# Optimization experiments

Hardware: AMD Instinct MI355X
Metric: run time of the kernel (lower is better)

Reference implementation:

```python
import jax, jax.numpy as jnp
import numpy as np

HIDDEN = 512
LATENT = 256
NUM_NODE_TYPES = 16


def setup_inputs() -> dict:
    key = jax.random.key(0)
    ks = jax.random.split(key, 9)
    s = lambda fan_in: 1.0 / np.sqrt(fan_in)
    return {
        "z": jax.random.normal(ks[0], (1024, LATENT), dtype=jnp.float32),
        "num_nodes": 128,
        "W_z": jax.random.uniform(ks[1], (LATENT, HIDDEN), jnp.float32, -s(LATENT), s(LATENT)),
        "b_z": jax.random.uniform(ks[2], (HIDDEN,), jnp.float32, -s(LATENT), s(LATENT)),
        "W_node": jax.random.uniform(ks[3], (HIDDEN, NUM_NODE_TYPES), jnp.float32, -s(HIDDEN), s(HIDDEN)),
        "b_node": jax.random.uniform(ks[4], (NUM_NODE_TYPES,), jnp.float32, -s(HIDDEN), s(HIDDEN)),
        "W_e1": jax.random.uniform(ks[5], (2 * HIDDEN, HIDDEN), jnp.float32, -s(2 * HIDDEN), s(2 * HIDDEN)),
        "b_e1": jax.random.uniform(ks[6], (HIDDEN,), jnp.float32, -s(2 * HIDDEN), s(2 * HIDDEN)),
        "W_e2": jax.random.uniform(ks[7], (HIDDEN, 1), jnp.float32, -s(HIDDEN), s(HIDDEN)),
        "b_e2": jax.random.uniform(ks[8], (1,), jnp.float32, -s(HIDDEN), s(HIDDEN)),
    }


def reference(z, num_nodes, W_z, b_z, W_node, b_node, W_e1, b_e1, W_e2, b_e2):
    # h: [B, H]
    h = jax.nn.relu(z @ W_z + b_z)
    B = z.shape[0]
    # h_expanded: [B, N, H] (same h replicated per node, as in the original)
    h_expanded = jnp.broadcast_to(h[:, None, :], (B, num_nodes, h.shape[-1]))
    node_logits = h_expanded @ W_node + b_node  # [B, N, T]
    # Every (i, j) pair in the original loop uses cat(h, h) -> identical scalar per batch.
    h_pair = jnp.concatenate([h, h], axis=-1)  # [B, 2H]
    p = jax.nn.sigmoid(jax.nn.relu(h_pair @ W_e1 + b_e1) @ W_e2 + b_e2)  # [B, 1]
    # Scatter onto strict lower triangle (j < i), zeros elsewhere.
    tril = jnp.tril(jnp.ones((num_nodes, num_nodes), dtype=z.dtype), k=-1)  # [N, N]
    edge_probs = p[:, :, None] * tril[None, :, :]  # [B, N, N]
    return node_logits, edge_probs
```

## Files before the change

kernel.cpp:

```cpp
#include <hip/hip_runtime.h>
#include <hip/hip_bf16.h>
#include <math.h>

#define BB 1024
#define LL 256
#define HH 512
#define TT 16
#define NN 128

#define NODE_F4 (BB * NN * TT / 4)
#define EDGE_F4 (BB * NN * NN / 4)

typedef short bf16x8 __attribute__((ext_vector_type(8)));
typedef short s16x4  __attribute__((ext_vector_type(4)));
typedef float f32x4  __attribute__((ext_vector_type(4)));

static __device__ __forceinline__ short bfbits(float f) {
    __hip_bfloat16 h = __float2bfloat16(f);
    return *reinterpret_cast<short*>(&h);
}

__device__ __forceinline__ void transpose_tile(const float* __restrict__ in,
                                               __hip_bfloat16* __restrict__ out,
                                               int k0, int n0, int Kdim, bool fold,
                                               __hip_bfloat16 (*tile)[34]) {
    const int tx = threadIdx.x & 31;
    const int ty = threadIdx.x >> 5;
    #pragma unroll
    for (int r = ty; r < 32; r += 8) {
        float v = in[(k0 + r) * HH + n0 + tx];
        if (fold) v += in[(k0 + r + HH) * HH + n0 + tx];
        tile[r][tx] = __float2bfloat16(v);
    }
    __syncthreads();
    #pragma unroll
    for (int r = ty; r < 32; r += 8) {
        out[(n0 + r) * Kdim + k0 + tx] = tile[tx][r];
    }
}

__global__ __launch_bounds__(256) void k_prep(const float* __restrict__ z,
                                              const float* __restrict__ Wz,
                                              const float* __restrict__ We1,
                                              const float* __restrict__ Wn,
                                              __hip_bfloat16* __restrict__ z_bf,
                                              __hip_bfloat16* __restrict__ WzT,
                                              __hip_bfloat16* __restrict__ WsumT,
                                              __hip_bfloat16* __restrict__ WnT,
                                              float* __restrict__ p_acc) {
    __shared__ __hip_bfloat16 tile[32][34];
    const int bid = blockIdx.x;
    const int tid = threadIdx.x;
    if (bid < 256) {
        const int q = bid * 256 + tid;
        float4 v = ((const float4*)z)[q];
        s16x4 o; o.x = bfbits(v.x); o.y = bfbits(v.y); o.z = bfbits(v.z); o.w = bfbits(v.w);
        ((s16x4*)z_bf)[q] = o;
    } else if (bid < 384) {
        const int t = bid - 256;
        transpose_tile(Wz, WzT, (t >> 4) * 32, (t & 15) * 32, LL, false, tile);
    } else if (bid < 640) {
        const int t = bid - 384;
        transpose_tile(We1, WsumT, (t >> 4) * 32, (t & 15) * 32, HH, true, tile);
    } else if (bid < 672) {
        const int u = (bid - 640) * 256 + tid;
        const int tt = u >> 9, k = u & 511;
        WnT[u] = __float2bfloat16(Wn[k * TT + tt]);
    } else {
        ((float4*)p_acc)[tid] = make_float4(0.f, 0.f, 0.f, 0.f);
    }
}

__global__ __launch_bounds__(256) void k_gemm1(const __hip_bfloat16* __restrict__ A,
                                               const __hip_bfloat16* __restrict__ Bt,
                                               const float* __restrict__ bias,
                                               __hip_bfloat16* __restrict__ out) {
    const int wid  = (blockIdx.x << 2) + (threadIdx.x >> 6);
    const int lane = threadIdx.x & 63;
    const int mt = wid >> 5, nt = wid & 31;
    const int l16 = lane & 15, quad = lane >> 4;

    const short* Ap = (const short*)A  + (mt * 16 + l16) * LL + quad * 8;
    const short* Bp = (const short*)Bt + (nt * 16 + l16) * LL + quad * 8;

    f32x4 acc = {0.f, 0.f, 0.f, 0.f};
    #pragma unroll
    for (int kt = 0; kt < LL / 32; ++kt) {
        bf16x8 a = *(const bf16x8*)(Ap + kt * 32);
        bf16x8 b = *(const bf16x8*)(Bp + kt * 32);
        acc = __builtin_amdgcn_mfma_f32_16x16x32_bf16(a, b, acc, 0, 0, 0);
    }
    const int col = nt * 16 + l16;
    const float bb = bias[col];
    #pragma unroll
    for (int r = 0; r < 4; ++r) {
        out[(mt * 16 + quad * 4 + r) * HH + col] = __float2bfloat16(fmaxf(acc[r] + bb, 0.f));
    }
}

__global__ __launch_bounds__(256) void k_gemm2_phead(const __hip_bfloat16* __restrict__ A,
                                                     const __hip_bfloat16* __restrict__ Bt,
                                                     const float* __restrict__ be1,
                                                     const float* __restrict__ We2,
                                                     float* __restrict__ p_acc) {
    const int wid  = (blockIdx.x << 2) + (threadIdx.x >> 6);
    const int lane = threadIdx.x & 63;
    const int mt = wid >> 5, nt = wid & 31;
    const int l16 = lane & 15, quad = lane >> 4;

    const short* Ap = (const short*)A  + (mt * 16 + l16) * HH + quad * 8;
    const short* Bp = (const short*)Bt + (nt * 16 + l16) * HH + quad * 8;

    f32x4 acc = {0.f, 0.f, 0.f, 0.f};
    #pragma unroll
    for (int kt = 0; kt < HH / 32; ++kt) {
        bf16x8 a = *(const bf16x8*)(Ap + kt * 32);
        bf16x8 b = *(const bf16x8*)(Bp + kt * 32);
        acc = __builtin_amdgcn_mfma_f32_16x16x32_bf16(a, b, acc, 0, 0, 0);
    }
    const int col = nt * 16 + l16;
    const float bb = be1[col];
    const float w2 = We2[col];
    float sr[4];
    #pragma unroll
    for (int r = 0; r < 4; ++r) sr[r] = fmaxf(acc[r] + bb, 0.f) * w2;
    #pragma unroll
    for (int off = 1; off < 16; off <<= 1) {
        #pragma unroll
        for (int r = 0; r < 4; ++r) sr[r] += __shfl_xor(sr[r], off);
    }
    if (l16 == 0) {
        #pragma unroll
        for (int r = 0; r < 4; ++r)
            atomicAdd(p_acc + mt * 16 + quad * 4 + r, sr[r]);
    }
}

__global__ __launch_bounds__(256) void k_small(const __hip_bfloat16* __restrict__ h,
                                               const __hip_bfloat16* __restrict__ WnT,
                                               const float* __restrict__ bn,
                                               const float* __restrict__ p_acc,
                                               const float* __restrict__ be2,
                                               float* __restrict__ node16,
                                               float* __restrict__ p) {
    const int wid  = (blockIdx.x << 2) + (threadIdx.x >> 6);
    const int lane = threadIdx.x & 63;
    const int l16 = lane & 15, quad = lane >> 4;

    const short* Ap = (const short*)h   + (wid * 16 + l16) * HH + quad * 8;
    const short* Bp = (const short*)WnT + l16 * HH + quad * 8;

    f32x4 acc = {0.f, 0.f, 0.f, 0.f};
    #pragma unroll
    for (int kt = 0; kt < HH / 32; ++kt) {
        bf16x8 a = *(const bf16x8*)(Ap + kt * 32);
        bf16x8 b = *(const bf16x8*)(Bp + kt * 32);
        acc = __builtin_amdgcn_mfma_f32_16x16x32_bf16(a, b, acc, 0, 0, 0);
    }
    const float bb = bn[l16];
    #pragma unroll
    for (int r = 0; r < 4; ++r)
        node16[(wid * 16 + quad * 4 + r) * TT + l16] = acc[r] + bb;

    const int idx = blockIdx.x * 256 + threadIdx.x;
    if (idx < BB) {
        float t = p_acc[idx] + be2[0];
        p[idx] = 1.f / (1.f + expf(-t));
    }
}

__global__ __launch_bounds__(256) void k_write(const float* __restrict__ node16,
                                               const float* __restrict__ p,
                                               float4* __restrict__ out) {
    const int q = blockIdx.x * 256 + threadIdx.x;
    if (q < NODE_F4) {
        const int b  = q >> 9;
        const int t4 = q & 3;
        out[q] = ((const float4*)(node16 + b * TT))[t4];
    } else {
        const int e  = q - NODE_F4;
        const int b  = e >> 12;
        const int i  = (e >> 5) & 127;
        const int j0 = (e & 31) * 4;
        const float pv = p[b];
        float4 v;
        v.x = (j0 + 0 < i) ? pv : 0.f;
        v.y = (j0 + 1 < i) ? pv : 0.f;
        v.z = (j0 + 2 < i) ? pv : 0.f;
        v.w = (j0 + 3 < i) ? pv : 0.f;
        out[q] = v;
    }
}

extern "C" void kernel_launch(void* const* d_in, const int* in_sizes, int n_in,
                              void* d_out, int out_size, void* d_ws, size_t ws_size,
                              hipStream_t stream) {
    const float* z    = (const float*)d_in[0];
    const float* Wz   = (const float*)d_in[2];
    const float* bz   = (const float*)d_in[3];
    const float* Wn   = (const float*)d_in[4];
    const float* bn   = (const float*)d_in[5];
    const float* We1  = (const float*)d_in[6];
    const float* be1  = (const float*)d_in[7];
    const float* We2  = (const float*)d_in[8];
    const float* be2  = (const float*)d_in[9];
    float* out = (float*)d_out;

    char* base = (char*)d_ws;
    __hip_bfloat16* z_bf   = (__hip_bfloat16*)(base);
    __hip_bfloat16* WzT    = (__hip_bfloat16*)(base +  512 * 1024);
    __hip_bfloat16* WsumT  = (__hip_bfloat16*)(base +  768 * 1024);
    __hip_bfloat16* WnT    = (__hip_bfloat16*)(base + 1280 * 1024);
    __hip_bfloat16* h_bf   = (__hip_bfloat16*)(base + 1296 * 1024);
    float*          node16 = (float*)(base + 2320 * 1024);
    float*          p_acc  = (float*)(base + 2384 * 1024);
    float*          p      = (float*)(base + 2388 * 1024);

    k_prep<<<673, 256, 0, stream>>>(z, Wz, We1, Wn, z_bf, WzT, WsumT, WnT, p_acc);

    k_gemm1<<<512, 256, 0, stream>>>(z_bf, WzT, bz, h_bf);

    k_gemm2_phead<<<512, 256, 0, stream>>>(h_bf, WsumT, be1, We2, p_acc);

    k_small<<<16, 256, 0, stream>>>(h_bf, WnT, bn, p_acc, be2, node16, p);

    k_write<<<(NODE_F4 + EDGE_F4) / 256, 256, 0, stream>>>(node16, p, (float4*)out);

    (void)in_sizes; (void)n_in; (void)out_size; (void)ws_size;
}
```

Baseline: 128.6 us.

## Fuse both GEMMs, node head and edge head into one per-row-tile kernel

Replaces the separate z-to-bf16 conversion, GEMM1, GEMM2+p-head and small node-head kernels with one kernel. Each 512-thread block owns 16 batch rows, converts z to bf16 in registers, computes h into a swizzled LDS buffer, then runs the node-logit and edge-MLP GEMMs from LDS and reduces partial sums in shared memory instead of with global atomics. This removes three launches, the global round trip for h and z_bf, and the p_acc zeroing and atomics. In exchange only 64 blocks run, so far fewer waves occupy the GPU, and every block re-reads the full weight matrices.

```diff
diff --git a/kernel.cpp b/kernel.cpp
--- a/kernel.cpp
+++ b/kernel.cpp
@@ -12,12 +12,15 @@
 #define EDGE_F4 (BB * NN * NN / 4)
 
 typedef short bf16x8 __attribute__((ext_vector_type(8)));
-typedef short s16x4  __attribute__((ext_vector_type(4)));
 typedef float f32x4  __attribute__((ext_vector_type(4)));
 
 static __device__ __forceinline__ short bfbits(float f) {
     __hip_bfloat16 h = __float2bfloat16(f);
     return *reinterpret_cast<short*>(&h);
+}
+
+static __device__ __forceinline__ int h_addr(int row, int col) {
+    return (row << 10) + ((((col >> 3) ^ (row & 7)) << 4)) + ((col & 7) << 1);
 }
 
 __device__ __forceinline__ void transpose_tile(const float* __restrict__ in,
@@ -39,133 +42,148 @@
     }
 }
 
-__global__ __launch_bounds__(256) void k_prep(const float* __restrict__ z,
-                                              const float* __restrict__ Wz,
+__global__ __launch_bounds__(256) void k_prep(const float* __restrict__ Wz,
                                               const float* __restrict__ We1,
                                               const float* __restrict__ Wn,
-                                              __hip_bfloat16* __restrict__ z_bf,
                                               __hip_bfloat16* __restrict__ WzT,
                                               __hip_bfloat16* __restrict__ WsumT,
-                                              __hip_bfloat16* __restrict__ WnT,
-                                              float* __restrict__ p_acc) {
+                                              __hip_bfloat16* __restrict__ WnT) {
     __shared__ __hip_bfloat16 tile[32][34];
     const int bid = blockIdx.x;
     const int tid = threadIdx.x;
-    if (bid < 256) {
-        const int q = bid * 256 + tid;
-        float4 v = ((const float4*)z)[q];
-        s16x4 o; o.x = bfbits(v.x); o.y = bfbits(v.y); o.z = bfbits(v.z); o.w = bfbits(v.w);
-        ((s16x4*)z_bf)[q] = o;
+    if (bid < 128) {
+        transpose_tile(Wz, WzT, (bid >> 4) * 32, (bid & 15) * 32, LL, false, tile);
     } else if (bid < 384) {
-        const int t = bid - 256;
-        transpose_tile(Wz, WzT, (t >> 4) * 32, (t & 15) * 32, LL, false, tile);
-    } else if (bid < 640) {
-        const int t = bid - 384;
+        const int t = bid - 128;
         transpose_tile(We1, WsumT, (t >> 4) * 32, (t & 15) * 32, HH, true, tile);
-    } else if (bid < 672) {
-        const int u = (bid - 640) * 256 + tid;
+    } else {
+        const int u = (bid - 384) * 256 + tid;
         const int tt = u >> 9, k = u & 511;
         WnT[u] = __float2bfloat16(Wn[k * TT + tt]);
-    } else {
-        ((float4*)p_acc)[tid] = make_float4(0.f, 0.f, 0.f, 0.f);
-    }
-}
-
-__global__ __launch_bounds__(256) void k_gemm1(const __hip_bfloat16* __restrict__ A,
-                                               const __hip_bfloat16* __restrict__ Bt,
-                                               const float* __restrict__ bias,
-                                               __hip_bfloat16* __restrict__ out) {
-    const int wid  = (blockIdx.x << 2) + (threadIdx.x >> 6);
-    const int lane = threadIdx.x & 63;
-    const int mt = wid >> 5, nt = wid & 31;
-    const int l16 = lane & 15, quad = lane >> 4;
-
-    const short* Ap = (const short*)A  + (mt * 16 + l16) * LL + quad * 8;
-    const short* Bp = (const short*)Bt + (nt * 16 + l16) * LL + quad * 8;
-
-    f32x4 acc = {0.f, 0.f, 0.f, 0.f};
-    #pragma unroll
-    for (int kt = 0; kt < LL / 32; ++kt) {
-        bf16x8 a = *(const bf16x8*)(Ap + kt * 32);
-        bf16x8 b = *(const bf16x8*)(Bp + kt * 32);
-        acc = __builtin_amdgcn_mfma_f32_16x16x32_bf16(a, b, acc, 0, 0, 0);
-    }
-    const int col = nt * 16 + l16;
-    const float bb = bias[col];
-    #pragma unroll
-    for (int r = 0; r < 4; ++r) {
-        out[(mt * 16 + quad * 4 + r) * HH + col] = __float2bfloat16(fmaxf(acc[r] + bb, 0.f));
-    }
-}
-
-__global__ __launch_bounds__(256) void k_gemm2_phead(const __hip_bfloat16* __restrict__ A,
-                                                     const __hip_bfloat16* __restrict__ Bt,
-                                                     const float* __restrict__ be1,
-                                                     const float* __restrict__ We2,
-                                                     float* __restrict__ p_acc) {
-    const int wid  = (blockIdx.x << 2) + (threadIdx.x >> 6);
-    const int lane = threadIdx.x & 63;
-    const int mt = wid >> 5, nt = wid & 31;
-    const int l16 = lane & 15, quad = lane >> 4;
-
-    const short* Ap = (const short*)A  + (mt * 16 + l16) * HH + quad * 8;
-    const short* Bp = (const short*)Bt + (nt * 16 + l16) * HH + quad * 8;
-
-    f32x4 acc = {0.f, 0.f, 0.f, 0.f};
-    #pragma unroll
-    for (int kt = 0; kt < HH / 32; ++kt) {
-        bf16x8 a = *(const bf16x8*)(Ap + kt * 32);
-        bf16x8 b = *(const bf16x8*)(Bp + kt * 32);
-        acc = __builtin_amdgcn_mfma_f32_16x16x32_bf16(a, b, acc, 0, 0, 0);
-    }
-    const int col = nt * 16 + l16;
-    const float bb = be1[col];
-    const float w2 = We2[col];
-    float sr[4];
-    #pragma unroll
-    for (int r = 0; r < 4; ++r) sr[r] = fmaxf(acc[r] + bb, 0.f) * w2;
-    #pragma unroll
-    for (int off = 1; off < 16; off <<= 1) {
-        #pragma unroll
-        for (int r = 0; r < 4; ++r) sr[r] += __shfl_xor(sr[r], off);
-    }
-    if (l16 == 0) {
-        #pragma unroll
-        for (int r = 0; r < 4; ++r)
-            atomicAdd(p_acc + mt * 16 + quad * 4 + r, sr[r]);
-    }
-}
-
-__global__ __launch_bounds__(256) void k_small(const __hip_bfloat16* __restrict__ h,
+    }
+}
+
+__global__ __launch_bounds__(512) void k_fused(const float* __restrict__ z,
+                                               const __hip_bfloat16* __restrict__ WzT,
+                                               const __hip_bfloat16* __restrict__ WsumT,
                                                const __hip_bfloat16* __restrict__ WnT,
+                                               const float* __restrict__ bz,
+                                               const float* __restrict__ be1,
+                                               const float* __restrict__ We2,
                                                const float* __restrict__ bn,
-                                               const float* __restrict__ p_acc,
                                                const float* __restrict__ be2,
                                                float* __restrict__ node16,
                                                float* __restrict__ p) {
-    const int wid  = (blockIdx.x << 2) + (threadIdx.x >> 6);
+    __shared__ char  hbuf[16384];
+    __shared__ f32x4 nod_lds[8][64];
+    __shared__ float pw_lds[8][16];
+
+    const int w    = threadIdx.x >> 6;
     const int lane = threadIdx.x & 63;
-    const int l16 = lane & 15, quad = lane >> 4;
-
-    const short* Ap = (const short*)h   + (wid * 16 + l16) * HH + quad * 8;
-    const short* Bp = (const short*)WnT + l16 * HH + quad * 8;
-
-    f32x4 acc = {0.f, 0.f, 0.f, 0.f};
+    const int l16  = lane & 15, quad = lane >> 4;
+    const int r0   = blockIdx.x << 4;
+
+    bf16x8 afr[8];
+    {
+        const float4* zf = (const float4*)(z + (r0 + l16) * LL);
+        #pragma unroll
+        for (int kt = 0; kt < 8; ++kt) {
+            float4 v0 = zf[quad * 2 + kt * 8];
+            float4 v1 = zf[quad * 2 + kt * 8 + 1];
+            bf16x8 a;
+            a[0] = bfbits(v0.x); a[1] = bfbits(v0.y); a[2] = bfbits(v0.z); a[3] = bfbits(v0.w);
+            a[4] = bfbits(v1.x); a[5] = bfbits(v1.y); a[6] = bfbits(v1.z); a[7] = bfbits(v1.w);
+            afr[kt] = a;
+        }
+    }
     #pragma unroll
-    for (int kt = 0; kt < HH / 32; ++kt) {
-        bf16x8 a = *(const bf16x8*)(Ap + kt * 32);
-        bf16x8 b = *(const bf16x8*)(Bp + kt * 32);
-        acc = __builtin_amdgcn_mfma_f32_16x16x32_bf16(a, b, acc, 0, 0, 0);
-    }
-    const float bb = bn[l16];
-    #pragma unroll
-    for (int r = 0; r < 4; ++r)
-        node16[(wid * 16 + quad * 4 + r) * TT + l16] = acc[r] + bb;
-
-    const int idx = blockIdx.x * 256 + threadIdx.x;
-    if (idx < BB) {
-        float t = p_acc[idx] + be2[0];
-        p[idx] = 1.f / (1.f + expf(-t));
+    for (int i = 0; i < 4; ++i) {
+        const int nt = (w << 2) + i;
+        const short* Bp = (const short*)WzT + (nt * 16 + l16) * LL + quad * 8;
+        f32x4 acc = {0.f, 0.f, 0.f, 0.f};
+        #pragma unroll
+        for (int kt = 0; kt < 8; ++kt) {
+            bf16x8 b = *(const bf16x8*)(Bp + kt * 32);
+            acc = __builtin_amdgcn_mfma_f32_16x16x32_bf16(afr[kt], b, acc, 0, 0, 0);
+        }
+        const int col = nt * 16 + l16;
+        const float bb = bz[col];
+        #pragma unroll
+        for (int r = 0; r < 4; ++r) {
+            float hv = fmaxf(acc[r] + bb, 0.f);
+            *(short*)(hbuf + h_addr(quad * 4 + r, col)) = bfbits(hv);
+        }
+    }
+    __syncthreads();
+
+    {
+        f32x4 acc = {0.f, 0.f, 0.f, 0.f};
+        const short* Bp = (const short*)WnT + l16 * HH + quad * 8;
+        #pragma unroll
+        for (int kk = 0; kk < 2; ++kk) {
+            const int kt = w * 2 + kk;
+            bf16x8 a = *(const bf16x8*)(hbuf + h_addr(l16, quad * 8 + kt * 32));
+            bf16x8 b = *(const bf16x8*)(Bp + kt * 32);
+            acc = __builtin_amdgcn_mfma_f32_16x16x32_bf16(a, b, acc, 0, 0, 0);
+        }
+        nod_lds[w][lane] = acc;
+    }
+
+    {
+        f32x4 acc[4];
+        #pragma unroll
+        for (int i = 0; i < 4; ++i) acc[i] = (f32x4){0.f, 0.f, 0.f, 0.f};
+        #pragma unroll
+        for (int kt = 0; kt < 16; ++kt) {
+            bf16x8 a = *(const bf16x8*)(hbuf + h_addr(l16, quad * 8 + kt * 32));
+            #pragma unroll
+            for (int i = 0; i < 4; ++i) {
+                const int nt = (w << 2) + i;
+                bf16x8 b = *(const bf16x8*)((const short*)WsumT +
+                            (nt * 16 + l16) * HH + quad * 8 + kt * 32);
+                acc[i] = __builtin_amdgcn_mfma_f32_16x16x32_bf16(a, b, acc[i], 0, 0, 0);
+            }
+        }
+        float psum[4] = {0.f, 0.f, 0.f, 0.f};
+        #pragma unroll
+        for (int i = 0; i < 4; ++i) {
+            const int col = ((w << 2) + i) * 16 + l16;
+            const float bb = be1[col], w2 = We2[col];
+            float sr[4];
+            #pragma unroll
+            for (int r = 0; r < 4; ++r) sr[r] = fmaxf(acc[i][r] + bb, 0.f) * w2;
+            #pragma unroll
+            for (int off = 1; off < 16; off <<= 1) {
+                #pragma unroll
+                for (int r = 0; r < 4; ++r) sr[r] += __shfl_xor(sr[r], off);
+            }
+            #pragma unroll
+            for (int r = 0; r < 4; ++r) psum[r] += sr[r];
+        }
+        if (l16 == 0) {
+            #pragma unroll
+            for (int r = 0; r < 4; ++r) pw_lds[w][quad * 4 + r] = psum[r];
+        }
+    }
+    __syncthreads();
+
+    if (w == 0) {
+        f32x4 s = nod_lds[0][lane];
+        #pragma unroll
+        for (int ww = 1; ww < 8; ++ww) {
+            f32x4 t = nod_lds[ww][lane];
+            s[0] += t[0]; s[1] += t[1]; s[2] += t[2]; s[3] += t[3];
+        }
+        const float bb = bn[l16];
+        #pragma unroll
+        for (int r = 0; r < 4; ++r)
+            node16[(r0 + quad * 4 + r) * TT + l16] = s[r] + bb;
+    } else if (w == 1 && lane < 16) {
+        float t = 0.f;
+        #pragma unroll
+        for (int ww = 0; ww < 8; ++ww) t += pw_lds[ww][lane];
+        t += be2[0];
+        p[r0 + lane] = 1.f / (1.f + expf(-t));
     }
 }
 
@@ -207,22 +225,16 @@
     float* out = (float*)d_out;
 
     char* base = (char*)d_ws;
-    __hip_bfloat16* z_bf   = (__hip_bfloat16*)(base);
-    __hip_bfloat16* WzT    = (__hip_bfloat16*)(base +  512 * 1024);
-    __hip_bfloat16* WsumT  = (__hip_bfloat16*)(base +  768 * 1024);
-    __hip_bfloat16* WnT    = (__hip_bfloat16*)(base + 1280 * 1024);
-    __hip_bfloat16* h_bf   = (__hip_bfloat16*)(base + 1296 * 1024);
-    float*          node16 = (float*)(base + 2320 * 1024);
-    float*          p_acc  = (float*)(base + 2384 * 1024);
-    float*          p      = (float*)(base + 2388 * 1024);
-
-    k_prep<<<673, 256, 0, stream>>>(z, Wz, We1, Wn, z_bf, WzT, WsumT, WnT, p_acc);
-
-    k_gemm1<<<512, 256, 0, stream>>>(z_bf, WzT, bz, h_bf);
-
-    k_gemm2_phead<<<512, 256, 0, stream>>>(h_bf, WsumT, be1, We2, p_acc);
-
-    k_small<<<16, 256, 0, stream>>>(h_bf, WnT, bn, p_acc, be2, node16, p);
+    __hip_bfloat16* WzT    = (__hip_bfloat16*)(base);
+    __hip_bfloat16* WsumT  = (__hip_bfloat16*)(base +  256 * 1024);
+    __hip_bfloat16* WnT    = (__hip_bfloat16*)(base +  768 * 1024);
+    float*          node16 = (float*)(base + 784 * 1024);
+    float*          p      = (float*)(base + 848 * 1024);
+
+    k_prep<<<416, 256, 0, stream>>>(Wz, We1, Wn, WzT, WsumT, WnT);
+
+    k_fused<<<BB / 16, 512, 0, stream>>>(z, WzT, WsumT, WnT,
+                                         bz, be1, We2, bn, be2, node16, p);
 
     k_write<<<(NODE_F4 + EDGE_F4) / 256, 256, 0, stream>>>(node16, p, (float4*)out);
 
```

Result: slower. 134.5 us (+4.6%).
